# Optimization experiments

Measured on AMD Instinct MI355X. Metric: run time of the kernel, lower is better.

Reference implementation:

```python
import jax, jax.numpy as jnp
import numpy as np

# Model hyperparameters (match init_kwargs)
D_MODEL = 1024
D_STATE = 16
D_CONV = 4
EXPAND = 2
NUM_BLOCKS = 4
D_INNER = EXPAND * D_MODEL            # 2048
DT_RANK = (D_MODEL + 15) // 16        # 64 (math.ceil(d_model/16), Mamba default)
BATCH, SEQLEN = 2, 1024


def setup_inputs() -> dict:
    key = jax.random.key(0)
    ks = jax.random.split(key, 16)
    s = 0.02  # init scale for random weights
    inp = {
        "x": jax.random.normal(ks[0], (BATCH, SEQLEN), jnp.float32),
        # embedding: nn.Linear(1, d_model)
        "emb_w": jax.random.normal(ks[1], (D_MODEL, 1), jnp.float32) * s,
        "emb_b": jax.random.normal(ks[2], (D_MODEL,), jnp.float32) * s,
        # per-block Mamba params, stacked on leading num_blocks axis
        "in_proj_w": jax.random.normal(ks[3], (NUM_BLOCKS, 2 * D_INNER, D_MODEL), jnp.float32) * s,
        "conv_w": jax.random.normal(ks[4], (NUM_BLOCKS, D_INNER, D_CONV), jnp.float32) * s,
        "conv_b": jax.random.normal(ks[5], (NUM_BLOCKS, D_INNER), jnp.float32) * s,
        "x_proj_w": jax.random.normal(ks[6], (NUM_BLOCKS, DT_RANK + 2 * D_STATE, D_INNER), jnp.float32) * s,
        "dt_proj_w": jax.random.normal(ks[7], (NUM_BLOCKS, D_INNER, DT_RANK), jnp.float32) * s,
        "dt_proj_b": jax.random.normal(ks[8], (NUM_BLOCKS, D_INNER), jnp.float32) * s,
        # A = -exp(A_log); standard S4D-real init: A_log = log(1..d_state)
        "A_log": jnp.broadcast_to(
            jnp.log(jnp.arange(1, D_STATE + 1, dtype=jnp.float32)),
            (NUM_BLOCKS, D_INNER, D_STATE)).copy(),
        "D_param": jnp.ones((NUM_BLOCKS, D_INNER), jnp.float32),
        "out_proj_w": jax.random.normal(ks[9], (NUM_BLOCKS, D_MODEL, D_INNER), jnp.float32) * s,
    }
    return inp


def _mamba_block(h, in_w, cw, cb, xp_w, dt_w, dt_b, A_log, Dp, out_w):
    B, L, _ = h.shape
    xz = jnp.einsum("bld,ed->ble", h, in_w)          # [B,L,2*Di]
    xx, z = jnp.split(xz, 2, axis=-1)                  # each [B,L,Di]

    # causal depthwise conv1d (padding=d_conv-1, truncated to L)
    xpad = jnp.pad(xx, ((0, 0), (D_CONV - 1, 0), (0, 0)))
    xc = cb
    for k in range(D_CONV):
        xc = xc + cw[:, k] * jax.lax.dynamic_slice_in_dim(xpad, k, L, axis=1)
    u = jax.nn.silu(xc)                                 # [B,L,Di]

    x_dbl = jnp.einsum("bld,ed->ble", u, xp_w)        # [B,L,dt_rank+2N]
    dt_lo = x_dbl[..., :DT_RANK]
    Bm = x_dbl[..., DT_RANK:DT_RANK + D_STATE]         # [B,L,N]
    Cm = x_dbl[..., DT_RANK + D_STATE:]                # [B,L,N]
    dt = jax.nn.softplus(jnp.einsum("blr,dr->bld", dt_lo, dt_w) + dt_b)  # [B,L,Di]

    A = -jnp.exp(A_log)                                 # [Di,N]

    def step(hst, ins):
        dt_t, B_t, C_t, u_t = ins                       # [B,Di],[B,N],[B,N],[B,Di]
        dA = jnp.exp(dt_t[:, :, None] * A)              # [B,Di,N]
        hst = dA * hst + (dt_t * u_t)[:, :, None] * B_t[:, None, :]
        y_t = jnp.einsum("bdn,bn->bd", hst, C_t)
        return hst, y_t

    xs = (dt.transpose(1, 0, 2), Bm.transpose(1, 0, 2),
          Cm.transpose(1, 0, 2), u.transpose(1, 0, 2))
    h0 = jnp.zeros((B, D_INNER, D_STATE), h.dtype)
    _, ys = jax.lax.scan(step, h0, xs)                  # [L,B,Di]
    y = ys.transpose(1, 0, 2) + Dp * u                  # skip term D*u
    y = y * jax.nn.silu(z)                              # gated
    return jnp.einsum("bld,ed->ble", y, out_w)        # [B,L,D]


def reference(x, emb_w, emb_b, in_proj_w, conv_w, conv_b, x_proj_w,
              dt_proj_w, dt_proj_b, A_log, D_param, out_proj_w):
    # embedding: Linear(1 -> d_model) on x.unsqueeze(-1)
    h = x[..., None] * emb_w[:, 0] + emb_b              # [B,L,D]
    for i in range(NUM_BLOCKS):
        h = _mamba_block(h, in_proj_w[i], conv_w[i], conv_b[i], x_proj_w[i],
                         dt_proj_w[i], dt_proj_b[i], A_log[i], D_param[i],
                         out_proj_w[i])
        h = jax.nn.silu(h)                               # activation after each block
    return h
```

## Files before the change

kernel.cpp:

```cpp
#include <hip/hip_runtime.h>
#include <math.h>

#define D_MODEL  1024
#define D_STATE  16
#define D_CONV   4
#define D_INNER  2048
#define DT_RANK  64
#define NUM_BLK  4
#define BATCH    2
#define SEQLEN   1024
#define ML       (BATCH*SEQLEN)
#define XPROJ_N  (DT_RANK + 2*D_STATE)
#define CH       32
#define CL       32
#define KSPL     16
#define KSEG     (D_INNER / KSPL)

typedef __attribute__((ext_vector_type(8))) short short8;
typedef __attribute__((ext_vector_type(4))) float f32x4;

__device__ __forceinline__ float silu_f(float x) {
    return x / (1.0f + __expf(-x));
}
__device__ __forceinline__ float softplus_f(float x) {
    if (x > 15.0f) return x;
    return __logf(1.0f + __expf(x));
}
__device__ __forceinline__ unsigned short f2bf(float x) {
    unsigned int u = __float_as_uint(x);
    u += 0x7FFFu + ((u >> 16) & 1u);
    return (unsigned short)(u >> 16);
}
__device__ __forceinline__ float bf2f(unsigned short h) {
    return __uint_as_float(((unsigned int)h) << 16);
}

__global__ __launch_bounds__(256) void embed_kernel(
    const float* __restrict__ x, const float* __restrict__ ew,
    const float* __restrict__ eb,
    unsigned short* __restrict__ h_hi, unsigned short* __restrict__ h_lo)
{
    int t  = blockIdx.x * 256 + threadIdx.x;
    int d  = t & (D_MODEL - 1);
    int bl = t >> 10;
    float v = fmaf(x[bl], ew[d], eb[d]);
    unsigned short h16 = f2bf(v);
    h_hi[t] = h16;
    h_lo[t] = f2bf(v - bf2f(h16));
}

__global__ __launch_bounds__(256) void tobf16_kernel(
    const float* __restrict__ src, unsigned short* __restrict__ dst, int n4)
{
    int t = blockIdx.x * 256 + threadIdx.x;
    if (t >= n4) return;
    float4 v = ((const float4*)src)[t];
    ushort4 h;
    h.x = f2bf(v.x); h.y = f2bf(v.y); h.z = f2bf(v.z); h.w = f2bf(v.w);
    ((ushort4*)dst)[t] = h;
}

template<int BM, int BN, int WM, int WN, int EPI>
__global__ __launch_bounds__(WM*WN*64) void mfma_gemm(
    const unsigned short* __restrict__ Ahi, const unsigned short* __restrict__ Alo,
    const unsigned short* __restrict__ Whi,
    float* __restrict__ Cf, unsigned short* __restrict__ Chi,
    unsigned short* __restrict__ Clo,
    int M, int N, int K)
{
    constexpr int NW  = WM * WN;
    constexpr int WTM = BM / WM;
    constexpr int WTN = BN / WN;
    constexpr int MT  = WTM / 16;
    constexpr int NT  = WTN / 16;
    constexpr int NCH = (2*BM + BN) / 16;
    constexpr int CPW = NCH / NW;

    __shared__ unsigned short lds[(2*BM + BN) * 32];

    const int tid  = threadIdx.x;
    const int wave = tid >> 6;
    const int lane = tid & 63;
    const int m0 = blockIdx.y * BM;
    const int n0 = blockIdx.x * BN;
    const int wm0 = (wave % WM) * WTM;
    const int wn0 = (wave / WM) * WTN;
    const int lrow = lane & 15;
    const int kqi  = lane >> 4;

    const int rc = lane >> 2;
    const int po = ((lane & 3) - (rc >> 1)) & 3;

    const unsigned short* gsrc[CPW];
    unsigned short* ldst[CPW];
    #pragma unroll
    for (int cc = 0; cc < CPW; cc++) {
        int c  = wave * CPW + cc;
        int r0 = c * 16;
        const unsigned short* s; int row;
        if      (r0 < BM)        { s = Ahi; row = m0 + r0; }
        else if (r0 < 2*BM)      { s = Alo; row = m0 + r0 - BM; }
        else                     { s = Whi; row = n0 + r0 - 2*BM; }
        gsrc[cc] = s + (size_t)(row + rc) * K + po * 8;
        ldst[cc] = &lds[c * 512];
    }

    f32x4 acc[MT][NT] = {};

    for (int kt = 0; kt < K; kt += 32) {
        __syncthreads();
        #pragma unroll
        for (int cc = 0; cc < CPW; cc++)
            __builtin_amdgcn_global_load_lds(
                (const __attribute__((address_space(1))) unsigned int*)(gsrc[cc] + kt),
                (__attribute__((address_space(3))) unsigned int*)ldst[cc],
                16, 0, 0);
        asm volatile("s_waitcnt vmcnt(0)" ::: "memory");
        __syncthreads();

        short8 ahi[MT], alo[MT], bhi[NT];
        #pragma unroll
        for (int i = 0; i < MT; i++) {
            int r = wm0 + i * 16 + lrow;
            int o = (kqi + ((r >> 1) & 3)) & 3;
            ahi[i] = *(const short8*)&lds[r * 32 + o * 8];
            alo[i] = *(const short8*)&lds[(BM + r) * 32 + o * 8];
        }
        #pragma unroll
        for (int j = 0; j < NT; j++) {
            int r = wn0 + j * 16 + lrow;
            int o = (kqi + ((r >> 1) & 3)) & 3;
            bhi[j] = *(const short8*)&lds[(2*BM + r) * 32 + o * 8];
        }
        #pragma unroll
        for (int i = 0; i < MT; i++)
            #pragma unroll
            for (int j = 0; j < NT; j++) {
                acc[i][j] = __builtin_amdgcn_mfma_f32_16x16x32_bf16(ahi[i], bhi[j], acc[i][j], 0, 0, 0);
                acc[i][j] = __builtin_amdgcn_mfma_f32_16x16x32_bf16(alo[i], bhi[j], acc[i][j], 0, 0, 0);
            }
    }

    const int orow = (lane >> 4) * 4;
    #pragma unroll
    for (int i = 0; i < MT; i++) {
        #pragma unroll
        for (int j = 0; j < NT; j++) {
            #pragma unroll
            for (int r = 0; r < 4; r++) {
                int gm = m0 + wm0 + i * 16 + orow + r;
                int gn = n0 + wn0 + j * 16 + lrow;
                size_t off = (size_t)gm * N + gn;
                float v = acc[i][j][r];
                if (EPI == 0) {
                    Cf[off] = v;
                } else if (EPI == 1) {
                    Cf[off] = silu_f(v);
                } else {
                    float s = silu_f(v);
                    unsigned short h16 = f2bf(s);
                    Chi[off] = h16;
                    Clo[off] = f2bf(s - bf2f(h16));
                }
            }
        }
    }
}

template <int ACT>
__global__ __launch_bounds__(256) void gemm_nt(
    const float* __restrict__ A, int lda,
    const float* __restrict__ W, int ldw,
    const float* __restrict__ bias,
    float* __restrict__ C, int ldc,
    int M, int N, int K)
{
    const int BM = 64, BN = 64, BK = 16;
    __shared__ float As[BK][BM + 4];
    __shared__ float Ws[BK][BN + 4];

    int tid = threadIdx.x;
    int bx  = blockIdx.x;
    int by  = blockIdx.y;
    int tx  = tid & 15;
    int ty  = tid >> 4;

    int lr = tid >> 2;
    int lk = (tid & 3) * 4;

    int am = by * BM + lr;
    int wn = bx * BN + lr;
    bool wok = (wn < N);

    const float* Ap = A + (size_t)am * lda + lk;
    const float* Wp = wok ? (W + (size_t)wn * ldw + lk) : W;

    float acc[4][4] = {};

    for (int kt = 0; kt < K; kt += BK) {
        float4 av = *(const float4*)(Ap + kt);
        float4 wv = wok ? *(const float4*)(Wp + kt) : make_float4(0.f,0.f,0.f,0.f);

        __syncthreads();
        As[lk+0][lr] = av.x; As[lk+1][lr] = av.y;
        As[lk+2][lr] = av.z; As[lk+3][lr] = av.w;
        Ws[lk+0][lr] = wv.x; Ws[lk+1][lr] = wv.y;
        Ws[lk+2][lr] = wv.z; Ws[lk+3][lr] = wv.w;
        __syncthreads();

        #pragma unroll
        for (int k = 0; k < BK; k++) {
            float4 a = *(const float4*)&As[k][ty*4];
            float4 b = *(const float4*)&Ws[k][tx*4];
            float ar[4] = {a.x, a.y, a.z, a.w};
            float br[4] = {b.x, b.y, b.z, b.w};
            #pragma unroll
            for (int i = 0; i < 4; i++)
                #pragma unroll
                for (int j = 0; j < 4; j++)
                    acc[i][j] = fmaf(ar[i], br[j], acc[i][j]);
        }
    }

    int m0 = by * BM + ty * 4;
    int n0 = bx * BN + tx * 4;
    #pragma unroll
    for (int i = 0; i < 4; i++) {
        #pragma unroll
        for (int j = 0; j < 4; j++) {
            int n = n0 + j;
            if (n < N) {
                float v = acc[i][j];
                if (ACT == 1) v = softplus_f(v + bias[n]);
                C[(size_t)(m0 + i) * ldc + n] = v;
            }
        }
    }
}

__global__ __launch_bounds__(256) void xproj_splitk(
    const float* __restrict__ xz, const float* __restrict__ cw,
    const float* __restrict__ cb, const float* __restrict__ W,
    float* __restrict__ P)
{
    const int BM = 64, BN = 64, BK = 16;
    __shared__ float As[BK][BM + 4];
    __shared__ float Ws[BK][BN + 4];

    int tid = threadIdx.x;
    int bx  = blockIdx.x;
    int by  = blockIdx.y;
    int kz  = blockIdx.z;
    int tx  = tid & 15;
    int ty  = tid >> 4;

    int lr = tid >> 2;
    int lk = (tid & 3) * 4;

    int am = by * BM + lr;
    int l  = am & (SEQLEN - 1);
    int wn = bx * BN + lr;
    bool wok = (wn < XPROJ_N);

    const float* Ap3 = xz + (size_t)am * (2 * D_INNER) + lk;
    bool g2 = (l >= 1), g1 = (l >= 2), g0 = (l >= 3);
    const float* Ap2 = Ap3 - (g2 ? 1 : 0) * (2 * D_INNER);
    const float* Ap1 = Ap3 - (g1 ? 2 : 0) * (2 * D_INNER);
    const float* Ap0 = Ap3 - (g0 ? 3 : 0) * (2 * D_INNER);
    const float* Wp  = wok ? (W + (size_t)wn * D_INNER + lk) : W;

    float acc[4][4] = {};

    for (int kt = kz * KSEG; kt < (kz + 1) * KSEG; kt += BK) {
        int k = kt + lk;
        float4 x3 = *(const float4*)(Ap3 + kt);
        float4 x2 = *(const float4*)(Ap2 + kt);
        float4 x1 = *(const float4*)(Ap1 + kt);
        float4 x0 = *(const float4*)(Ap0 + kt);
        if (!g2) x2 = make_float4(0.f,0.f,0.f,0.f);
        if (!g1) x1 = make_float4(0.f,0.f,0.f,0.f);
        if (!g0) x0 = make_float4(0.f,0.f,0.f,0.f);
        float4 c0 = *(const float4*)(cw + (k+0) * 4);
        float4 c1 = *(const float4*)(cw + (k+1) * 4);
        float4 c2 = *(const float4*)(cw + (k+2) * 4);
        float4 c3 = *(const float4*)(cw + (k+3) * 4);
        float4 cbv = *(const float4*)(cb + k);
        float4 av;
        av.x = silu_f(cbv.x + c0.x*x0.x + c0.y*x1.x + c0.z*x2.x + c0.w*x3.x);
        av.y = silu_f(cbv.y + c1.x*x0.y + c1.y*x1.y + c1.z*x2.y + c1.w*x3.y);
        av.z = silu_f(cbv.z + c2.x*x0.z + c2.y*x1.z + c2.z*x2.z + c2.w*x3.z);
        av.w = silu_f(cbv.w + c3.x*x0.w + c3.y*x1.w + c3.z*x2.w + c3.w*x3.w);
        float4 wv = wok ? *(const float4*)(Wp + kt) : make_float4(0.f,0.f,0.f,0.f);

        __syncthreads();
        As[lk+0][lr] = av.x; As[lk+1][lr] = av.y;
        As[lk+2][lr] = av.z; As[lk+3][lr] = av.w;
        Ws[lk+0][lr] = wv.x; Ws[lk+1][lr] = wv.y;
        Ws[lk+2][lr] = wv.z; Ws[lk+3][lr] = wv.w;
        __syncthreads();

        #pragma unroll
        for (int kk = 0; kk < BK; kk++) {
            float4 a = *(const float4*)&As[kk][ty*4];
            float4 b = *(const float4*)&Ws[kk][tx*4];
            float ar[4] = {a.x, a.y, a.z, a.w};
            float br[4] = {b.x, b.y, b.z, b.w};
            #pragma unroll
            for (int i = 0; i < 4; i++)
                #pragma unroll
                for (int j = 0; j < 4; j++)
                    acc[i][j] = fmaf(ar[i], br[j], acc[i][j]);
        }
    }

    float* Pz = P + (size_t)kz * ML * XPROJ_N;
    int m0 = by * BM + ty * 4;
    int n0 = bx * BN + tx * 4;
    #pragma unroll
    for (int i = 0; i < 4; i++) {
        #pragma unroll
        for (int j = 0; j < 4; j++) {
            int n = n0 + j;
            if (n < XPROJ_N)
                Pz[(size_t)(m0 + i) * XPROJ_N + n] = acc[i][j];
        }
    }
}

__global__ __launch_bounds__(256) void xproj_reduce(
    const float* __restrict__ P, float* __restrict__ xd)
{
    int t = blockIdx.x * 256 + threadIdx.x;
    float4 s = ((const float4*)P)[t];
    #pragma unroll
    for (int z = 1; z < KSPL; z++) {
        float4 v = ((const float4*)(P + (size_t)z * ML * XPROJ_N))[t];
        s.x += v.x; s.y += v.y; s.z += v.z; s.w += v.w;
    }
    ((float4*)xd)[t] = s;
}

__global__ __launch_bounds__(256) void scan_pass1(
    const float* __restrict__ dt, const float* __restrict__ xz,
    const float* __restrict__ xdbl, const float* __restrict__ cw,
    const float* __restrict__ cb, const float* __restrict__ A_log,
    float* __restrict__ s_arr, float* __restrict__ sdt_arr)
{
    int d = blockIdx.x * 256 + threadIdx.x;
    int j = blockIdx.y;
    int b = blockIdx.z;

    float Av[D_STATE];
    #pragma unroll
    for (int n = 0; n < D_STATE; n++)
        Av[n] = -__expf(A_log[d * D_STATE + n]);

    float4 cwv = *(const float4*)(cw + d * 4);
    float cbd = cb[d];

    float st[D_STATE] = {};
    float sdt = 0.f;

    size_t idx = ((size_t)(b * SEQLEN + j * CL)) * D_INNER + d;
    size_t xxi = ((size_t)(b * SEQLEN + j * CL)) * (2 * D_INNER) + d;
    const float* xr = xdbl + (size_t)(b * SEQLEN + j * CL) * XPROJ_N + DT_RANK;

    float w0 = 0.f, w1 = 0.f, w2 = 0.f;
    if (j) {
        w0 = xz[xxi - 3 * (2 * D_INNER)];
        w1 = xz[xxi - 2 * (2 * D_INNER)];
        w2 = xz[xxi - 1 * (2 * D_INNER)];
    }

    for (int l = 0; l < CL; l++) {
        float w3 = xz[xxi];
        float uv = silu_f(fmaf(cwv.w, w3, fmaf(cwv.z, w2,
                     fmaf(cwv.y, w1, fmaf(cwv.x, w0, cbd)))));
        float dtv = dt[idx];
        float du  = dtv * uv;
        sdt += dtv;
        float4 B0 = *(const float4*)(xr + 0);
        float4 B1 = *(const float4*)(xr + 4);
        float4 B2 = *(const float4*)(xr + 8);
        float4 B3 = *(const float4*)(xr + 12);
        float Bv[16] = {B0.x,B0.y,B0.z,B0.w, B1.x,B1.y,B1.z,B1.w,
                        B2.x,B2.y,B2.z,B2.w, B3.x,B3.y,B3.z,B3.w};
        #pragma unroll
        for (int n = 0; n < D_STATE; n++)
            st[n] = fmaf(st[n], __expf(dtv * Av[n]), du * Bv[n]);
        w0 = w1; w1 = w2; w2 = w3;
        idx += D_INNER;
        xxi += 2 * D_INNER;
        xr  += XPROJ_N;
    }

    size_t base = (size_t)(b * CH + j) * D_STATE * D_INNER + d;
    #pragma unroll
    for (int n = 0; n < D_STATE; n++)
        s_arr[base + (size_t)n * D_INNER] = st[n];
    sdt_arr[(size_t)(b * CH + j) * D_INNER + d] = sdt;
}

__global__ __launch_bounds__(256) void scan_pass2(
    const float* __restrict__ A_log, const float* __restrict__ sdt_arr,
    float* __restrict__ s_arr)
{
    int t = blockIdx.x * 256 + threadIdx.x;
    int d = t & (D_INNER - 1);
    int n = (t >> 11) & (D_STATE - 1);
    int b = t >> 15;

    float Av = -__expf(A_log[d * D_STATE + n]);
    float init = 0.f;
    for (int j = 0; j < CH; j++) {
        size_t off = ((size_t)(b * CH + j) * D_STATE + n) * D_INNER + d;
        float sv  = s_arr[off];
        float sdt = sdt_arr[(size_t)(b * CH + j) * D_INNER + d];
        s_arr[off] = init;
        init = fmaf(init, __expf(Av * sdt), sv);
    }
}

__global__ __launch_bounds__(256) void scan_pass3(
    const float* __restrict__ dt, const float* __restrict__ xz,
    const float* __restrict__ xdbl, const float* __restrict__ cw,
    const float* __restrict__ cb, const float* __restrict__ A_log,
    const float* __restrict__ Dp, const float* __restrict__ s_arr,
    unsigned short* __restrict__ y_hi, unsigned short* __restrict__ y_lo)
{
    int d = blockIdx.x * 256 + threadIdx.x;
    int j = blockIdx.y;
    int b = blockIdx.z;

    float Av[D_STATE];
    #pragma unroll
    for (int n = 0; n < D_STATE; n++)
        Av[n] = -__expf(A_log[d * D_STATE + n]);
    float Dd = Dp[d];
    float4 cwv = *(const float4*)(cw + d * 4);
    float cbd = cb[d];

    float st[D_STATE];
    size_t sbase = (size_t)(b * CH + j) * D_STATE * D_INNER + d;
    #pragma unroll
    for (int n = 0; n < D_STATE; n++)
        st[n] = s_arr[sbase + (size_t)n * D_INNER];

    size_t idx = ((size_t)(b * SEQLEN + j * CL)) * D_INNER + d;
    size_t xxi = ((size_t)(b * SEQLEN + j * CL)) * (2 * D_INNER) + d;
    const float* xr = xdbl + (size_t)(b * SEQLEN + j * CL) * XPROJ_N + DT_RANK;

    float w0 = 0.f, w1 = 0.f, w2 = 0.f;
    if (j) {
        w0 = xz[xxi - 3 * (2 * D_INNER)];
        w1 = xz[xxi - 2 * (2 * D_INNER)];
        w2 = xz[xxi - 1 * (2 * D_INNER)];
    }

    for (int l = 0; l < CL; l++) {
        float w3 = xz[xxi];
        float uv = silu_f(fmaf(cwv.w, w3, fmaf(cwv.z, w2,
                     fmaf(cwv.y, w1, fmaf(cwv.x, w0, cbd)))));
        float dtv = dt[idx];
        float du  = dtv * uv;
        float4 B0 = *(const float4*)(xr + 0);
        float4 B1 = *(const float4*)(xr + 4);
        float4 B2 = *(const float4*)(xr + 8);
        float4 B3 = *(const float4*)(xr + 12);
        float4 C0 = *(const float4*)(xr + 16);
        float4 C1 = *(const float4*)(xr + 20);
        float4 C2 = *(const float4*)(xr + 24);
        float4 C3 = *(const float4*)(xr + 28);
        float Bv[16] = {B0.x,B0.y,B0.z,B0.w, B1.x,B1.y,B1.z,B1.w,
                        B2.x,B2.y,B2.z,B2.w, B3.x,B3.y,B3.z,B3.w};
        float Cv[16] = {C0.x,C0.y,C0.z,C0.w, C1.x,C1.y,C1.z,C1.w,
                        C2.x,C2.y,C2.z,C2.w, C3.x,C3.y,C3.z,C3.w};
        float yt = 0.f;
        #pragma unroll
        for (int n = 0; n < D_STATE; n++) {
            float s = fmaf(st[n], __expf(dtv * Av[n]), du * Bv[n]);
            st[n] = s;
            yt = fmaf(s, Cv[n], yt);
        }
        float zv = xz[xxi + D_INNER];
        float yv = (yt + Dd * uv) * silu_f(zv);
        unsigned short h16 = f2bf(yv);
        y_hi[idx] = h16;
        y_lo[idx] = f2bf(yv - bf2f(h16));

        w0 = w1; w1 = w2; w2 = w3;
        idx += D_INNER;
        xxi += 2 * D_INNER;
        xr  += XPROJ_N;
    }
}

extern "C" void kernel_launch(void* const* d_in, const int* in_sizes, int n_in,
                              void* d_out, int out_size, void* d_ws, size_t ws_size,
                              hipStream_t stream)
{
    const float* x     = (const float*)d_in[0];
    const float* emb_w = (const float*)d_in[1];
    const float* emb_b = (const float*)d_in[2];
    const float* inw   = (const float*)d_in[3];
    const float* cw    = (const float*)d_in[4];
    const float* cb    = (const float*)d_in[5];
    const float* xpw   = (const float*)d_in[6];
    const float* dtw   = (const float*)d_in[7];
    const float* dtb   = (const float*)d_in[8];
    const float* Alog  = (const float*)d_in[9];
    const float* Dpar  = (const float*)d_in[10];
    const float* outw  = (const float*)d_in[11];

    float* out = (float*)d_out;

    float* ws    = (float*)d_ws;
    float* xz    = ws;
    float* xd    = xz + 8388608;
    float* dt    = xd + 196608;
    float* sdt   = dt + 4194304;
    float* s_arr = sdt + 131072;
    float* xpart = s_arr + 2097152;
    unsigned short* h_hi = (unsigned short*)(xpart + (size_t)KSPL * 196608);
    unsigned short* h_lo = h_hi + 2097152;
    unsigned short* y_hi = h_lo + 2097152;
    unsigned short* y_lo = y_hi + 4194304;
    unsigned short* wih  = y_lo + 4194304;
    unsigned short* woh  = wih + 4194304;

    embed_kernel<<<(ML * D_MODEL) / 256, 256, 0, stream>>>(x, emb_w, emb_b, h_hi, h_lo);

    for (int i = 0; i < NUM_BLK; i++) {
        const float* inw_i  = inw  + (size_t)i * (2 * D_INNER) * D_MODEL;
        const float* cw_i   = cw   + (size_t)i * D_INNER * D_CONV;
        const float* cb_i   = cb   + (size_t)i * D_INNER;
        const float* xpw_i  = xpw  + (size_t)i * XPROJ_N * D_INNER;
        const float* dtw_i  = dtw  + (size_t)i * D_INNER * DT_RANK;
        const float* dtb_i  = dtb  + (size_t)i * D_INNER;
        const float* Alog_i = Alog + (size_t)i * D_INNER * D_STATE;
        const float* Dp_i   = Dpar + (size_t)i * D_INNER;
        const float* outw_i = outw + (size_t)i * D_MODEL * D_INNER;

        tobf16_kernel<<<4096, 256, 0, stream>>>(inw_i, wih, 1048576);

        mfma_gemm<128, 128, 2, 4, 0><<<dim3(4096 / 128, 2048 / 128), 512, 0, stream>>>(
            h_hi, h_lo, wih, xz, nullptr, nullptr, ML, 2 * D_INNER, D_MODEL);

        xproj_splitk<<<dim3(2, ML / 64, KSPL), 256, 0, stream>>>(
            xz, cw_i, cb_i, xpw_i, xpart);
        xproj_reduce<<<(ML * XPROJ_N / 4) / 256, 256, 0, stream>>>(xpart, xd);

        gemm_nt<1><<<dim3(D_INNER / 64, ML / 64), 256, 0, stream>>>(
            xd, XPROJ_N, dtw_i, DT_RANK, dtb_i, dt, D_INNER,
            ML, D_INNER, DT_RANK);

        scan_pass1<<<dim3(D_INNER / 256, CH, BATCH), 256, 0, stream>>>(
            dt, xz, xd, cw_i, cb_i, Alog_i, s_arr, sdt);
        scan_pass2<<<(BATCH * D_INNER * D_STATE) / 256, 256, 0, stream>>>(
            Alog_i, sdt, s_arr);
        scan_pass3<<<dim3(D_INNER / 256, CH, BATCH), 256, 0, stream>>>(
            dt, xz, xd, cw_i, cb_i, Alog_i, Dp_i, s_arr, y_hi, y_lo);

        tobf16_kernel<<<2048, 256, 0, stream>>>(outw_i, woh, 524288);

        if (i == NUM_BLK - 1) {
            mfma_gemm<64, 128, 2, 4, 1><<<dim3(1024 / 128, 2048 / 64), 512, 0, stream>>>(
                y_hi, y_lo, woh, out, nullptr, nullptr, ML, D_MODEL, D_INNER);
        } else {
            mfma_gemm<64, 128, 2, 4, 2><<<dim3(1024 / 128, 2048 / 64), 512, 0, stream>>>(
                y_hi, y_lo, woh, nullptr, h_hi, h_lo, ML, D_MODEL, D_INNER);
        }
    }
}
```

Before: 869.8 us.

## Split-K the output projection GEMM and hoist weight bf16 conversion out of loop

The out-projection GEMM now splits K in two across blockIdx.z, writing partial sums into the xz scratch buffer. A new reduce kernel adds the partials, applies SiLU and emits the next block's bf16 hi/lo inputs or the final fp32 output. All four blocks' in/out weights are converted to bf16 in two batched launches up front instead of per block. This doubles the grid for the 256-block output GEMM to improve CU occupancy, at the cost of an extra fp32 round-trip through memory and a larger workspace for the pre-converted weights.

New measurement: 832.6 us. 4.3% less time.

```diff
diff --git a/kernel.cpp b/kernel.cpp
--- a/kernel.cpp
+++ b/kernel.cpp
@@ -60,7 +60,7 @@
     ((ushort4*)dst)[t] = h;
 }
 
-template<int BM, int BN, int WM, int WN, int EPI>
+template<int BM, int BN, int WM, int WN, int EPI, int KSPLIT>
 __global__ __launch_bounds__(WM*WN*64) void mfma_gemm(
     const unsigned short* __restrict__ Ahi, const unsigned short* __restrict__ Alo,
     const unsigned short* __restrict__ Whi,
@@ -107,7 +107,12 @@
 
     f32x4 acc[MT][NT] = {};
 
-    for (int kt = 0; kt < K; kt += 32) {
+    const int kseg = K / KSPLIT;
+    const int kz   = (KSPLIT > 1) ? blockIdx.z : 0;
+    const int kbeg = kz * kseg;
+    const int kend = kbeg + kseg;
+
+    for (int kt = kbeg; kt < kend; kt += 32) {
         __syncthreads();
         #pragma unroll
         for (int cc = 0; cc < CPW; cc++)
@@ -142,6 +147,7 @@
     }
 
     const int orow = (lane >> 4) * 4;
+    float* Cfz = Cf + (KSPLIT > 1 ? (size_t)kz * M * N : 0);
     #pragma unroll
     for (int i = 0; i < MT; i++) {
         #pragma unroll
@@ -152,8 +158,8 @@
                 int gn = n0 + wn0 + j * 16 + lrow;
                 size_t off = (size_t)gm * N + gn;
                 float v = acc[i][j][r];
-                if (EPI == 0) {
-                    Cf[off] = v;
+                if (KSPLIT > 1 || EPI == 0) {
+                    Cfz[off] = v;
                 } else if (EPI == 1) {
                     Cf[off] = silu_f(v);
                 } else {
@@ -164,6 +170,31 @@
                 }
             }
         }
+    }
+}
+
+template<int FINAL>
+__global__ __launch_bounds__(256) void oproj_reduce(
+    const float* __restrict__ P, float* __restrict__ outf,
+    unsigned short* __restrict__ hi, unsigned short* __restrict__ lo)
+{
+    const int MN4 = ML * D_MODEL / 4;
+    int t = blockIdx.x * 256 + threadIdx.x;
+    float4 a = ((const float4*)P)[t];
+    float4 b = ((const float4*)(P + (size_t)ML * D_MODEL))[t];
+    float4 s;
+    s.x = silu_f(a.x + b.x); s.y = silu_f(a.y + b.y);
+    s.z = silu_f(a.z + b.z); s.w = silu_f(a.w + b.w);
+    if (FINAL) {
+        ((float4*)outf)[t] = s;
+    } else {
+        ushort4 h, l;
+        h.x = f2bf(s.x); l.x = f2bf(s.x - bf2f(h.x));
+        h.y = f2bf(s.y); l.y = f2bf(s.y - bf2f(h.y));
+        h.z = f2bf(s.z); l.z = f2bf(s.z - bf2f(h.z));
+        h.w = f2bf(s.w); l.w = f2bf(s.w - bf2f(h.w));
+        ((ushort4*)hi)[t] = h;
+        ((ushort4*)lo)[t] = l;
     }
 }
 
@@ -525,13 +556,17 @@
     unsigned short* h_lo = h_hi + 2097152;
     unsigned short* y_hi = h_lo + 2097152;
     unsigned short* y_lo = y_hi + 4194304;
-    unsigned short* wih  = y_lo + 4194304;
-    unsigned short* woh  = wih + 4194304;
+    unsigned short* wih_all = y_lo + 4194304;
+    unsigned short* woh_all = wih_all + 4 * 4194304;
+
+    tobf16_kernel<<<(NUM_BLK * 1048576 + 255) / 256, 256, 0, stream>>>(
+        inw, wih_all, NUM_BLK * 1048576);
+    tobf16_kernel<<<(NUM_BLK * 524288 + 255) / 256, 256, 0, stream>>>(
+        outw, woh_all, NUM_BLK * 524288);
 
     embed_kernel<<<(ML * D_MODEL) / 256, 256, 0, stream>>>(x, emb_w, emb_b, h_hi, h_lo);
 
     for (int i = 0; i < NUM_BLK; i++) {
-        const float* inw_i  = inw  + (size_t)i * (2 * D_INNER) * D_MODEL;
         const float* cw_i   = cw   + (size_t)i * D_INNER * D_CONV;
         const float* cb_i   = cb   + (size_t)i * D_INNER;
         const float* xpw_i  = xpw  + (size_t)i * XPROJ_N * D_INNER;
@@ -539,11 +574,10 @@
         const float* dtb_i  = dtb  + (size_t)i * D_INNER;
         const float* Alog_i = Alog + (size_t)i * D_INNER * D_STATE;
         const float* Dp_i   = Dpar + (size_t)i * D_INNER;
-        const float* outw_i = outw + (size_t)i * D_MODEL * D_INNER;
-
-        tobf16_kernel<<<4096, 256, 0, stream>>>(inw_i, wih, 1048576);
-
-        mfma_gemm<128, 128, 2, 4, 0><<<dim3(4096 / 128, 2048 / 128), 512, 0, stream>>>(
+        unsigned short* wih = wih_all + (size_t)i * 4194304;
+        unsigned short* woh = woh_all + (size_t)i * 2097152;
+
+        mfma_gemm<128, 128, 2, 4, 0, 1><<<dim3(4096 / 128, 2048 / 128), 512, 0, stream>>>(
             h_hi, h_lo, wih, xz, nullptr, nullptr, ML, 2 * D_INNER, D_MODEL);
 
         xproj_splitk<<<dim3(2, ML / 64, KSPL), 256, 0, stream>>>(
@@ -561,14 +595,14 @@
         scan_pass3<<<dim3(D_INNER / 256, CH, BATCH), 256, 0, stream>>>(
             dt, xz, xd, cw_i, cb_i, Alog_i, Dp_i, s_arr, y_hi, y_lo);
 
-        tobf16_kernel<<<2048, 256, 0, stream>>>(outw_i, woh, 524288);
-
+        mfma_gemm<64, 128, 2, 4, 0, 2><<<dim3(1024 / 128, 2048 / 64, 2), 512, 0, stream>>>(
+            y_hi, y_lo, woh, xz, nullptr, nullptr, ML, D_MODEL, D_INNER);
         if (i == NUM_BLK - 1) {
-            mfma_gemm<64, 128, 2, 4, 1><<<dim3(1024 / 128, 2048 / 64), 512, 0, stream>>>(
-                y_hi, y_lo, woh, out, nullptr, nullptr, ML, D_MODEL, D_INNER);
+            oproj_reduce<1><<<(ML * D_MODEL / 4) / 256, 256, 0, stream>>>(
+                xz, out, nullptr, nullptr);
         } else {
-            mfma_gemm<64, 128, 2, 4, 2><<<dim3(1024 / 128, 2048 / 64), 512, 0, stream>>>(
-                y_hi, y_lo, woh, nullptr, h_hi, h_lo, ML, D_MODEL, D_INNER);
-        }
-    }
-}
+            oproj_reduce<0><<<(ML * D_MODEL / 4) / 256, 256, 0, stream>>>(
+                xz, nullptr, h_hi, h_lo);
+        }
+    }
+}
```
